# Kernel tuning notes

Measured on AMD Instinct MI355X. Metric: run time of the kernel, lower is better.

Reference implementation:

```python
import jax, jax.numpy as jnp
import numpy as np

MIN_NORM = 1e-15
N = 10000        # num_nodes
E = 320000       # num edges (avg degree 32)
F_IN = 512       # in_features
HID = 256        # hardcoded encoder hidden dim
D_HYP = 2        # Poincare embedding dim
HEIGHT = 2
MAX_SIZE = 0.999
MIN_SCALE = HEIGHT * (MAX_SIZE / (HEIGHT + 1))  # = 0.666, scale clamp lower bound
MAX_SCALE = MAX_SIZE


def setup_inputs() -> dict:
    key = jax.random.key(0)
    ks = jax.random.split(key, 5)
    feature = jax.random.normal(ks[0], (N, F_IN), jnp.float32)
    edge_index = jax.random.randint(ks[1], (2, E), 0, N, dtype=jnp.int64)
    W1 = jax.random.normal(ks[2], (F_IN, HID), jnp.float32) / np.sqrt(F_IN).astype(np.float32)
    b1 = jnp.zeros((HID,), jnp.float32)
    W2 = jax.random.normal(ks[3], (HID, D_HYP), jnp.float32) / np.sqrt(HID).astype(np.float32)
    b2 = jnp.zeros((D_HYP,), jnp.float32)
    scale = jnp.ones((1,), jnp.float32)  # init_size overridden to 1.0 in __init__
    return {"feature": feature, "edge_index": edge_index, "W1": W1, "b1": b1,
            "W2": W2, "b2": b2, "scale": scale}


def _gcn_agg(h, src, dst):
    # symmetric-normalized edge_index gather/aggregate (message passing)
    deg = jax.ops.segment_sum(jnp.ones((src.shape[0],), h.dtype), dst, num_segments=N)
    deg = jnp.maximum(deg, 1.0)
    norm = jax.lax.rsqrt(deg[src] * deg[dst])            # [E]
    msg = h[src] * norm[:, None]                          # [E, C] gather (irregular)
    return jax.ops.segment_sum(msg, dst, num_segments=N)  # [N, C] scatter-add


def reference(feature, edge_index, W1, b1, W2, b2, scale):
    src, dst = edge_index[0], edge_index[1]
    # 2-layer graph encoder (linear -> aggregate -> relu, linear -> aggregate)
    h = jax.nn.relu(_gcn_agg(feature @ W1 + b1, src, dst))   # [N, HID]
    u = _gcn_agg(h @ W2 + b2, src, dst)                      # [N, D_HYP] tangent at origin
    # lift to Lorentz model (k=-1) via expmap0: x = [cosh|u|, sinh|u| * u/|u|]
    un = jnp.maximum(jnp.linalg.norm(u, axis=-1, keepdims=True), MIN_NORM)
    x_l = jnp.concatenate([jnp.cosh(un), jnp.sinh(un) * u / un], axis=-1)  # [N, D_HYP+1]
    # Lorentz -> Poincare: p = x_space / (1 + x_time)
    p = x_l[:, 1:] / (1.0 + x_l[:, :1])
    # normalize: F.normalize(p, dim=-1) * scale.clamp(min_size, max_size)
    pn = jnp.maximum(jnp.linalg.norm(p, axis=-1, keepdims=True), 1e-12)
    s = jnp.clip(scale, MIN_SCALE, MAX_SCALE)
    p = p / pn * s
    # project onto Poincare ball of curvature k=-1 with eps=MIN_NORM
    norm = jnp.maximum(jnp.linalg.norm(p, axis=-1, keepdims=True), MIN_NORM)
    maxnorm = 1.0 - MIN_NORM
    return jnp.where(norm > maxnorm, p / norm * maxnorm, p)
```

## Files before the change

### kernel.cpp

```cpp
#include <hip/hip_runtime.h>
#include <math.h>

#define N_NODES 10000
#define N_EDGES 320000
#define F_IN 512
#define HID 256
#define PAD_DEG 80
#define N_GEMM_BLKS 632
#define BUILD_BLKS ((N_EDGES + 255) / 256)

typedef _Float16 half8 __attribute__((ext_vector_type(8)));
typedef float floatx4 __attribute__((ext_vector_type(4)));

typedef const __attribute__((address_space(1))) void* gas_ptr;
typedef __attribute__((address_space(3))) void* las_ptr;

__device__ __forceinline__ void dma16(const void* g, void* l) {
    __builtin_amdgcn_global_load_lds((gas_ptr)g, (las_ptr)l, 16, 0, 0);
}

__device__ __forceinline__ void fma4(float4& acc, float s, const float4& v) {
    acc.x += s * v.x; acc.y += s * v.y; acc.z += s * v.z; acc.w += s * v.w;
}


__global__ __launch_bounds__(256) void k_pre(const float* __restrict__ W1,
                                             int* __restrict__ count,
                                             _Float16* __restrict__ Bt_hi,
                                             _Float16* __restrict__ Bt_lo) {
    int i = blockIdx.x * blockDim.x + threadIdx.x;
    if (i < 10240) count[i] = 0;
    int k = i >> 8, n = i & 255;
    float v = W1[i];
    _Float16 hi = (_Float16)v;
    Bt_hi[n * F_IN + k] = hi;
    Bt_lo[n * F_IN + k] = (_Float16)(v - (float)hi);
}


__global__ __launch_bounds__(256) void k_main(const float* __restrict__ A,
                                              const _Float16* __restrict__ Bt_hi,
                                              const _Float16* __restrict__ Bt_lo,
                                              const float* __restrict__ b1,
                                              float* __restrict__ h0,
                                              const int* __restrict__ ei,
                                              int* __restrict__ count,
                                              int* __restrict__ csr) {
    __shared__ float    As[2][2048];
    __shared__ _Float16 Bhs[2][2048];
    __shared__ _Float16 Bls[2][2048];
    const int tid = threadIdx.x;

    if (blockIdx.x >= N_GEMM_BLKS) {
        int e = (blockIdx.x - N_GEMM_BLKS) * 256 + tid;
        if (e < N_EDGES) {
            int src = ei[e];
            int dst = ei[N_EDGES + e];
            int pos = atomicAdd(&count[dst], 1);
            csr[dst * PAD_DEG + pos] = src;
        }
        return;
    }

    const int b = blockIdx.x;
    const int t = (b & 7) * 79 + (b >> 3);
    const int row0 = (t >> 2) * 64, col0 = (t & 3) * 64;

    const int sA0 = tid, sA1 = tid + 256;
    const int rA0 = sA0 >> 3, hA0 = (sA0 & 7) ^ (rA0 & 7);
    const int rA1 = sA1 >> 3, hA1 = (sA1 & 7) ^ (rA1 & 7);
    int gr0 = row0 + rA0; if (gr0 > N_NODES - 1) gr0 = N_NODES - 1;
    int gr1 = row0 + rA1; if (gr1 > N_NODES - 1) gr1 = N_NODES - 1;
    const float* gA0 = A + (size_t)gr0 * F_IN + hA0 * 4;
    const float* gA1 = A + (size_t)gr1 * F_IN + hA1 * 4;
    const int cB = tid >> 2, hB = (tid & 3) ^ (cB & 3);
    const _Float16* gBh = Bt_hi + (size_t)(col0 + cB) * F_IN + hB * 8;
    const _Float16* gBl = Bt_lo + (size_t)(col0 + cB) * F_IN + hB * 8;

    const int wdma = __builtin_amdgcn_readfirstlane(tid >> 6);
    char* lA  = (char*)&As[0][0];
    char* lBh = (char*)&Bhs[0][0];
    char* lBl = (char*)&Bls[0][0];
    const int dA0u = wdma * 1024;
    const int dA1u = 4096 + wdma * 1024;
    const int dBu  = wdma * 1024;

    dma16(gA0, lA + dA0u);
    dma16(gA1, lA + dA1u);
    dma16(gBh, lBh + dBu);
    dma16(gBl, lBl + dBu);

    const int lane = tid & 63, w = tid >> 6;
    const int quad = lane >> 4, l15 = lane & 15;
    const int wm = (w >> 1) * 32, wn = (w & 1) * 32;
    floatx4 acc[2][2] = {};

    int aoff[2][2], boff[2];
    #pragma unroll
    for (int mi = 0; mi < 2; ++mi) {
        int r = wm + mi * 16 + l15;
        aoff[mi][0] = r * 128 + ((2 * quad)     ^ (r & 7)) * 16;
        aoff[mi][1] = r * 128 + ((2 * quad + 1) ^ (r & 7)) * 16;
    }
    #pragma unroll
    for (int ni = 0; ni < 2; ++ni) {
        int n = wn + ni * 16 + l15;
        boff[ni] = n * 64 + (quad ^ (n & 3)) * 16;
    }

    __syncthreads();

    int buf = 0;
    for (int it = 0; it < 16; ++it) {
        if (it < 15) {
            const int k1 = (it + 1) * 32;
            const int nb = buf ^ 1;
            dma16(gA0 + k1, lA  + nb * 8192 + dA0u);
            dma16(gA1 + k1, lA  + nb * 8192 + dA1u);
            dma16(gBh + k1, lBh + nb * 4096 + dBu);
            dma16(gBl + k1, lBl + nb * 4096 + dBu);
        }
        const char* bA = lA  + buf * 8192;
        const char* bH = lBh + buf * 4096;
        const char* bL = lBl + buf * 4096;
        half8 ah[2], al[2], bhf[2], blf[2];
        #pragma unroll
        for (int mi = 0; mi < 2; ++mi) {
            float4 f0 = *(const float4*)(bA + aoff[mi][0]);
            float4 f1 = *(const float4*)(bA + aoff[mi][1]);
            float av[8] = {f0.x, f0.y, f0.z, f0.w, f1.x, f1.y, f1.z, f1.w};
            #pragma unroll
            for (int j = 0; j < 8; ++j) {
                _Float16 h = (_Float16)av[j];
                ah[mi][j] = h;
                al[mi][j] = (_Float16)(av[j] - (float)h);
            }
        }
        #pragma unroll
        for (int ni = 0; ni < 2; ++ni) {
            bhf[ni] = *(const half8*)(bH + boff[ni]);
            blf[ni] = *(const half8*)(bL + boff[ni]);
        }
        #pragma unroll
        for (int ni = 0; ni < 2; ++ni)
            #pragma unroll
            for (int mi = 0; mi < 2; ++mi) {
                acc[mi][ni] = __builtin_amdgcn_mfma_f32_16x16x32_f16(ah[mi], bhf[ni], acc[mi][ni], 0, 0, 0);
                acc[mi][ni] = __builtin_amdgcn_mfma_f32_16x16x32_f16(ah[mi], blf[ni], acc[mi][ni], 0, 0, 0);
                acc[mi][ni] = __builtin_amdgcn_mfma_f32_16x16x32_f16(al[mi], bhf[ni], acc[mi][ni], 0, 0, 0);
            }
        __syncthreads();
        buf ^= 1;
    }

    #pragma unroll
    for (int mi = 0; mi < 2; ++mi)
        #pragma unroll
        for (int ni = 0; ni < 2; ++ni) {
            int colb = col0 + wn + ni * 16 + l15;
            float bias = b1[colb];
            #pragma unroll
            for (int reg = 0; reg < 4; ++reg) {
                int rowb = row0 + wm + mi * 16 + quad * 4 + reg;
                if (rowb < N_NODES) h0[(size_t)rowb * HID + colb] = acc[mi][ni][reg] + bias;
            }
        }
}


__global__ __launch_bounds__(256) void k_agg1(const float* __restrict__ h0,
                                              const int* __restrict__ csr,
                                              const int* __restrict__ count,
                                              const float* __restrict__ W2,
                                              const float* __restrict__ b2,
                                              float* __restrict__ u0) {
    __shared__ int2 nb[4][PAD_DEG];
    const int wid = threadIdx.x >> 6;
    const int lane = threadIdx.x & 63;
    const int n = blockIdx.x * 4 + wid;
    const int deg = count[n];
    const float degd = (float)(deg > 0 ? deg : 1);
    const int* row = csr + (size_t)n * PAD_DEG;
    for (int j = lane; j < deg; j += 64) {
        int s = row[j];
        int cs = count[s];
        float wq = rsqrtf((float)(cs > 0 ? cs : 1) * degd);
        nb[wid][j] = make_int2(s, __float_as_int(wq));
    }
    __syncthreads();

    const int off = lane << 2;
    float4 acc0 = {0,0,0,0}, acc1 = {0,0,0,0}, acc2 = {0,0,0,0}, acc3 = {0,0,0,0};
    int j = 0;
    for (; j + 16 <= deg; j += 16) {
        int2 e[16];
        #pragma unroll
        for (int q = 0; q < 16; ++q) e[q] = nb[wid][j + q];
        float4 v[16];
        #pragma unroll
        for (int q = 0; q < 16; ++q)
            v[q] = *(const float4*)(h0 + ((size_t)e[q].x << 8) + off);
        #pragma unroll
        for (int q = 0; q < 16; q += 4) {
            fma4(acc0, __int_as_float(e[q + 0].y), v[q + 0]);
            fma4(acc1, __int_as_float(e[q + 1].y), v[q + 1]);
            fma4(acc2, __int_as_float(e[q + 2].y), v[q + 2]);
            fma4(acc3, __int_as_float(e[q + 3].y), v[q + 3]);
        }
    }
    for (; j + 4 <= deg; j += 4) {
        int2 e0 = nb[wid][j+0], e1 = nb[wid][j+1], e2 = nb[wid][j+2], e3 = nb[wid][j+3];
        float4 v0 = *(const float4*)(h0 + ((size_t)e0.x << 8) + off);
        float4 v1 = *(const float4*)(h0 + ((size_t)e1.x << 8) + off);
        float4 v2 = *(const float4*)(h0 + ((size_t)e2.x << 8) + off);
        float4 v3 = *(const float4*)(h0 + ((size_t)e3.x << 8) + off);
        fma4(acc0, __int_as_float(e0.y), v0);
        fma4(acc1, __int_as_float(e1.y), v1);
        fma4(acc2, __int_as_float(e2.y), v2);
        fma4(acc3, __int_as_float(e3.y), v3);
    }
    for (; j < deg; ++j) {
        int2 e = nb[wid][j];
        float4 v = *(const float4*)(h0 + ((size_t)e.x << 8) + off);
        fma4(acc0, __int_as_float(e.y), v);
    }
    acc0.x += acc1.x + acc2.x + acc3.x;
    acc0.y += acc1.y + acc2.y + acc3.y;
    acc0.z += acc1.z + acc2.z + acc3.z;
    acc0.w += acc1.w + acc2.w + acc3.w;
    acc0.x = fmaxf(acc0.x, 0.f); acc0.y = fmaxf(acc0.y, 0.f);
    acc0.z = fmaxf(acc0.z, 0.f); acc0.w = fmaxf(acc0.w, 0.f);
    float4 wa = *(const float4*)(W2 + (lane << 3));
    float4 wb = *(const float4*)(W2 + (lane << 3) + 4);
    float p0 = acc0.x * wa.x + acc0.y * wa.z + acc0.z * wb.x + acc0.w * wb.z;
    float p1 = acc0.x * wa.y + acc0.y * wa.w + acc0.z * wb.y + acc0.w * wb.w;
    #pragma unroll
    for (int o = 32; o > 0; o >>= 1) {
        p0 += __shfl_down(p0, o);
        p1 += __shfl_down(p1, o);
    }
    if (lane == 0) {
        u0[2 * n]     = p0 + b2[0];
        u0[2 * n + 1] = p1 + b2[1];
    }
}


__global__ __launch_bounds__(256) void k_agg2(const float* __restrict__ u0,
                                              const int* __restrict__ csr,
                                              const int* __restrict__ count,
                                              const float* __restrict__ scale,
                                              float* __restrict__ out) {
    int n = blockIdx.x * 4 + (threadIdx.x >> 6);
    int lane = threadIdx.x & 63;
    if (n >= N_NODES) return;
    int deg = count[n];
    float degd = (float)(deg > 0 ? deg : 1);
    const int* row = csr + (size_t)n * PAD_DEG;
    float a0 = 0.f, a1 = 0.f;
    for (int j = lane; j < deg; j += 64) {
        int s = row[j];
        int cs = count[s];
        float wq = rsqrtf((float)(cs > 0 ? cs : 1) * degd);
        float2 uv = *(const float2*)(u0 + 2 * (size_t)s);
        a0 += wq * uv.x;
        a1 += wq * uv.y;
    }
    #pragma unroll
    for (int o = 32; o > 0; o >>= 1) {
        a0 += __shfl_down(a0, o);
        a1 += __shfl_down(a1, o);
    }
    if (lane == 0) {
        float un = fmaxf(sqrtf(a0 * a0 + a1 * a1), 1e-15f);
        float t = tanhf(0.5f * un) / un;
        float p0 = a0 * t, p1 = a1 * t;
        float pn = fmaxf(sqrtf(p0 * p0 + p1 * p1), 1e-12f);
        float s = fminf(fmaxf(scale[0], 0.666f), 0.999f);
        p0 = p0 / pn * s; p1 = p1 / pn * s;
        float nn = fmaxf(sqrtf(p0 * p0 + p1 * p1), 1e-15f);
        if (nn > 1.0f) { p0 = p0 / nn; p1 = p1 / nn; }
        out[2 * n]     = p0;
        out[2 * n + 1] = p1;
    }
}


extern "C" void kernel_launch(void* const* d_in, const int* in_sizes, int n_in,
                              void* d_out, int out_size, void* d_ws, size_t ws_size,
                              hipStream_t stream) {
    const float* feature = (const float*)d_in[0];
    const int*   ei      = (const int*)d_in[1];
    const float* W1      = (const float*)d_in[2];
    const float* b1      = (const float*)d_in[3];
    const float* W2      = (const float*)d_in[4];
    const float* b2      = (const float*)d_in[5];
    const float* scale   = (const float*)d_in[6];
    float* out = (float*)d_out;

    char* W = (char*)d_ws;
    int*      count = (int*)W;
    int*      csr   = (int*)(W + 40960);
    float*    h0    = (float*)(W + 3240960);
    float*    u0    = (float*)(W + 13480960);
    _Float16* Bt_hi = (_Float16*)(W + 13560960);
    _Float16* Bt_lo = (_Float16*)(W + 13823104);

    k_pre<<<dim3(512), dim3(256), 0, stream>>>(W1, count, Bt_hi, Bt_lo);
    k_main<<<dim3(N_GEMM_BLKS + BUILD_BLKS), dim3(256), 0, stream>>>(
        feature, Bt_hi, Bt_lo, b1, h0, ei, count, csr);
    k_agg1<<<dim3((N_NODES + 3) / 4), dim3(256), 0, stream>>>(h0, csr, count, W2, b2, u0);
    k_agg2<<<dim3((N_NODES + 3) / 4), dim3(256), 0, stream>>>(u0, csr, count, scale, out);
}
```

Before: 148.4 us.

## Fuse all stages into one cooperative persistent kernel with fp16 hidden activations

Replaces the four separate launches (weight split, GEMM+CSR build, layer-1 aggregation, layer-2 aggregation) with a single cooperative kernel of 512 blocks that uses grid.sync between phases. The GEMM tiles are distributed persistently, and the CSR build runs before the GEMM within each block. The hidden activation h0 is now stored as fp16, which halves the bytes touched by the irregular neighbour gather in layer 1. The aim is to cut launch gaps and gather bandwidth, in exchange for grid-wide barriers, reduced precision on h0, and the edge-build phase now serialised before the GEMM.

```diff
diff --git a/kernel.cpp b/kernel.cpp
--- a/kernel.cpp
+++ b/kernel.cpp
@@ -1,15 +1,20 @@
 #include <hip/hip_runtime.h>
+#include <hip/hip_cooperative_groups.h>
 #include <math.h>
+
+namespace cg = cooperative_groups;
 
 #define N_NODES 10000
 #define N_EDGES 320000
 #define F_IN 512
 #define HID 256
 #define PAD_DEG 80
-#define N_GEMM_BLKS 632
-#define BUILD_BLKS ((N_EDGES + 255) / 256)
+#define NBLK 512
+#define NWAVE (NBLK * 4)
+#define EDGES_PER_BLK 625
 
 typedef _Float16 half8 __attribute__((ext_vector_type(8)));
+typedef _Float16 half4v __attribute__((ext_vector_type(4)));
 typedef float floatx4 __attribute__((ext_vector_type(4)));
 
 typedef const __attribute__((address_space(1))) void* gas_ptr;
@@ -23,265 +28,267 @@
     acc.x += s * v.x; acc.y += s * v.y; acc.z += s * v.z; acc.w += s * v.w;
 }
 
-
-__global__ __launch_bounds__(256) void k_pre(const float* __restrict__ W1,
-                                             int* __restrict__ count,
-                                             _Float16* __restrict__ Bt_hi,
-                                             _Float16* __restrict__ Bt_lo) {
-    int i = blockIdx.x * blockDim.x + threadIdx.x;
-    if (i < 10240) count[i] = 0;
-    int k = i >> 8, n = i & 255;
-    float v = W1[i];
-    _Float16 hi = (_Float16)v;
-    Bt_hi[n * F_IN + k] = hi;
-    Bt_lo[n * F_IN + k] = (_Float16)(v - (float)hi);
-}
-
-
-__global__ __launch_bounds__(256) void k_main(const float* __restrict__ A,
-                                              const _Float16* __restrict__ Bt_hi,
-                                              const _Float16* __restrict__ Bt_lo,
-                                              const float* __restrict__ b1,
-                                              float* __restrict__ h0,
-                                              const int* __restrict__ ei,
-                                              int* __restrict__ count,
-                                              int* __restrict__ csr) {
+__device__ __forceinline__ float4 h4_to_f4(half4v h) {
+    float4 f; f.x = (float)h[0]; f.y = (float)h[1]; f.z = (float)h[2]; f.w = (float)h[3];
+    return f;
+}
+
+__global__ __launch_bounds__(256, 2) void k_fused(
+    const float* __restrict__ A, const int* __restrict__ ei,
+    const float* __restrict__ W1, const float* __restrict__ b1,
+    const float* __restrict__ W2, const float* __restrict__ b2,
+    const float* __restrict__ scale, float* __restrict__ out,
+    int* __restrict__ count, int* __restrict__ csr,
+    _Float16* __restrict__ h0h, float* __restrict__ u0,
+    _Float16* __restrict__ Bt_hi, _Float16* __restrict__ Bt_lo)
+{
     __shared__ float    As[2][2048];
     __shared__ _Float16 Bhs[2][2048];
     __shared__ _Float16 Bls[2][2048];
+    __shared__ int2     nb[4][PAD_DEG];
+
     const int tid = threadIdx.x;
-
-    if (blockIdx.x >= N_GEMM_BLKS) {
-        int e = (blockIdx.x - N_GEMM_BLKS) * 256 + tid;
-        if (e < N_EDGES) {
+    const int b = blockIdx.x;
+    const int lane = tid & 63, w = tid >> 6;
+    cg::grid_group grid = cg::this_grid();
+
+    {
+        int i = b * 256 + tid;
+        if (i < 10240) count[i] = 0;
+        int k = i >> 8, n = i & 255;
+        float v = W1[i];
+        _Float16 hi = (_Float16)v;
+        Bt_hi[n * F_IN + k] = hi;
+        Bt_lo[n * F_IN + k] = (_Float16)(v - (float)hi);
+    }
+    grid.sync();
+
+    {
+        const int e0 = b * EDGES_PER_BLK;
+        for (int j = tid; j < EDGES_PER_BLK; j += 256) {
+            int e = e0 + j;
             int src = ei[e];
             int dst = ei[N_EDGES + e];
             int pos = atomicAdd(&count[dst], 1);
             csr[dst * PAD_DEG + pos] = src;
         }
-        return;
-    }
-
-    const int b = blockIdx.x;
-    const int t = (b & 7) * 79 + (b >> 3);
-    const int row0 = (t >> 2) * 64, col0 = (t & 3) * 64;
-
-    const int sA0 = tid, sA1 = tid + 256;
-    const int rA0 = sA0 >> 3, hA0 = (sA0 & 7) ^ (rA0 & 7);
-    const int rA1 = sA1 >> 3, hA1 = (sA1 & 7) ^ (rA1 & 7);
-    int gr0 = row0 + rA0; if (gr0 > N_NODES - 1) gr0 = N_NODES - 1;
-    int gr1 = row0 + rA1; if (gr1 > N_NODES - 1) gr1 = N_NODES - 1;
-    const float* gA0 = A + (size_t)gr0 * F_IN + hA0 * 4;
-    const float* gA1 = A + (size_t)gr1 * F_IN + hA1 * 4;
-    const int cB = tid >> 2, hB = (tid & 3) ^ (cB & 3);
-    const _Float16* gBh = Bt_hi + (size_t)(col0 + cB) * F_IN + hB * 8;
-    const _Float16* gBl = Bt_lo + (size_t)(col0 + cB) * F_IN + hB * 8;
-
-    const int wdma = __builtin_amdgcn_readfirstlane(tid >> 6);
-    char* lA  = (char*)&As[0][0];
-    char* lBh = (char*)&Bhs[0][0];
-    char* lBl = (char*)&Bls[0][0];
-    const int dA0u = wdma * 1024;
-    const int dA1u = 4096 + wdma * 1024;
-    const int dBu  = wdma * 1024;
-
-    dma16(gA0, lA + dA0u);
-    dma16(gA1, lA + dA1u);
-    dma16(gBh, lBh + dBu);
-    dma16(gBl, lBl + dBu);
-
-    const int lane = tid & 63, w = tid >> 6;
-    const int quad = lane >> 4, l15 = lane & 15;
-    const int wm = (w >> 1) * 32, wn = (w & 1) * 32;
-    floatx4 acc[2][2] = {};
-
-    int aoff[2][2], boff[2];
-    #pragma unroll
-    for (int mi = 0; mi < 2; ++mi) {
-        int r = wm + mi * 16 + l15;
-        aoff[mi][0] = r * 128 + ((2 * quad)     ^ (r & 7)) * 16;
-        aoff[mi][1] = r * 128 + ((2 * quad + 1) ^ (r & 7)) * 16;
-    }
-    #pragma unroll
-    for (int ni = 0; ni < 2; ++ni) {
-        int n = wn + ni * 16 + l15;
-        boff[ni] = n * 64 + (quad ^ (n & 3)) * 16;
-    }
-
-    __syncthreads();
-
-    int buf = 0;
-    for (int it = 0; it < 16; ++it) {
-        if (it < 15) {
-            const int k1 = (it + 1) * 32;
-            const int nb = buf ^ 1;
-            dma16(gA0 + k1, lA  + nb * 8192 + dA0u);
-            dma16(gA1 + k1, lA  + nb * 8192 + dA1u);
-            dma16(gBh + k1, lBh + nb * 4096 + dBu);
-            dma16(gBl + k1, lBl + nb * 4096 + dBu);
-        }
-        const char* bA = lA  + buf * 8192;
-        const char* bH = lBh + buf * 4096;
-        const char* bL = lBl + buf * 4096;
-        half8 ah[2], al[2], bhf[2], blf[2];
+    }
+
+    {
+        const int quad = lane >> 4, l15 = lane & 15;
+        const int wm = (w >> 1) * 32, wn = (w & 1) * 32;
+        const int wdma = __builtin_amdgcn_readfirstlane(w);
+        char* lA  = (char*)&As[0][0];
+        char* lBh = (char*)&Bhs[0][0];
+        char* lBl = (char*)&Bls[0][0];
+        const int dA0u = wdma * 1024;
+        const int dA1u = 4096 + wdma * 1024;
+        const int dBu  = wdma * 1024;
+        const int sA0 = tid, sA1 = tid + 256;
+        const int rA0 = sA0 >> 3, hA0 = (sA0 & 7) ^ (rA0 & 7);
+        const int rA1 = sA1 >> 3, hA1 = (sA1 & 7) ^ (rA1 & 7);
+        const int cB = tid >> 2, hB = (tid & 3) ^ (cB & 3);
+        int aoff[2][2], boff[2];
         #pragma unroll
         for (int mi = 0; mi < 2; ++mi) {
-            float4 f0 = *(const float4*)(bA + aoff[mi][0]);
-            float4 f1 = *(const float4*)(bA + aoff[mi][1]);
-            float av[8] = {f0.x, f0.y, f0.z, f0.w, f1.x, f1.y, f1.z, f1.w};
-            #pragma unroll
-            for (int j = 0; j < 8; ++j) {
-                _Float16 h = (_Float16)av[j];
-                ah[mi][j] = h;
-                al[mi][j] = (_Float16)(av[j] - (float)h);
-            }
+            int r = wm + mi * 16 + l15;
+            aoff[mi][0] = r * 128 + ((2 * quad)     ^ (r & 7)) * 16;
+            aoff[mi][1] = r * 128 + ((2 * quad + 1) ^ (r & 7)) * 16;
         }
         #pragma unroll
         for (int ni = 0; ni < 2; ++ni) {
-            bhf[ni] = *(const half8*)(bH + boff[ni]);
-            blf[ni] = *(const half8*)(bL + boff[ni]);
-        }
-        #pragma unroll
-        for (int ni = 0; ni < 2; ++ni)
+            int nn = wn + ni * 16 + l15;
+            boff[ni] = nn * 64 + (quad ^ (nn & 3)) * 16;
+        }
+
+        const int ntile = (b < 116) ? 2 : 1;
+        for (int tt = 0; tt < ntile; ++tt) {
+            const int t = b + tt * 512;
+            const int row0 = (t >> 2) * 64, col0 = (t & 3) * 64;
+            int gr0 = row0 + rA0; if (gr0 > N_NODES - 1) gr0 = N_NODES - 1;
+            int gr1 = row0 + rA1; if (gr1 > N_NODES - 1) gr1 = N_NODES - 1;
+            const float* gA0 = A + (size_t)gr0 * F_IN + hA0 * 4;
+            const float* gA1 = A + (size_t)gr1 * F_IN + hA1 * 4;
+            const _Float16* gBh = Bt_hi + (size_t)(col0 + cB) * F_IN + hB * 8;
+            const _Float16* gBl = Bt_lo + (size_t)(col0 + cB) * F_IN + hB * 8;
+            floatx4 acc[2][2] = {};
+
+            dma16(gA0, lA + dA0u);
+            dma16(gA1, lA + dA1u);
+            dma16(gBh, lBh + dBu);
+            dma16(gBl, lBl + dBu);
+            __syncthreads();
+
+            int buf = 0;
+            for (int it = 0; it < 16; ++it) {
+                if (it < 15) {
+                    const int k1 = (it + 1) * 32;
+                    const int nbuf = buf ^ 1;
+                    dma16(gA0 + k1, lA  + nbuf * 8192 + dA0u);
+                    dma16(gA1 + k1, lA  + nbuf * 8192 + dA1u);
+                    dma16(gBh + k1, lBh + nbuf * 4096 + dBu);
+                    dma16(gBl + k1, lBl + nbuf * 4096 + dBu);
+                }
+                const char* bA = lA  + buf * 8192;
+                const char* bH = lBh + buf * 4096;
+                const char* bL = lBl + buf * 4096;
+                half8 ah[2], al[2], bhf[2], blf[2];
+                #pragma unroll
+                for (int mi = 0; mi < 2; ++mi) {
+                    float4 f0 = *(const float4*)(bA + aoff[mi][0]);
+                    float4 f1 = *(const float4*)(bA + aoff[mi][1]);
+                    float av[8] = {f0.x, f0.y, f0.z, f0.w, f1.x, f1.y, f1.z, f1.w};
+                    #pragma unroll
+                    for (int j = 0; j < 8; ++j) {
+                        _Float16 h = (_Float16)av[j];
+                        ah[mi][j] = h;
+                        al[mi][j] = (_Float16)(av[j] - (float)h);
+                    }
+                }
+                #pragma unroll
+                for (int ni = 0; ni < 2; ++ni) {
+                    bhf[ni] = *(const half8*)(bH + boff[ni]);
+                    blf[ni] = *(const half8*)(bL + boff[ni]);
+                }
+                #pragma unroll
+                for (int ni = 0; ni < 2; ++ni)
+                    #pragma unroll
+                    for (int mi = 0; mi < 2; ++mi) {
+                        acc[mi][ni] = __builtin_amdgcn_mfma_f32_16x16x32_f16(ah[mi], bhf[ni], acc[mi][ni], 0, 0, 0);
+                        acc[mi][ni] = __builtin_amdgcn_mfma_f32_16x16x32_f16(ah[mi], blf[ni], acc[mi][ni], 0, 0, 0);
+                        acc[mi][ni] = __builtin_amdgcn_mfma_f32_16x16x32_f16(al[mi], bhf[ni], acc[mi][ni], 0, 0, 0);
+                    }
+                __syncthreads();
+                buf ^= 1;
+            }
             #pragma unroll
-            for (int mi = 0; mi < 2; ++mi) {
-                acc[mi][ni] = __builtin_amdgcn_mfma_f32_16x16x32_f16(ah[mi], bhf[ni], acc[mi][ni], 0, 0, 0);
-                acc[mi][ni] = __builtin_amdgcn_mfma_f32_16x16x32_f16(ah[mi], blf[ni], acc[mi][ni], 0, 0, 0);
-                acc[mi][ni] = __builtin_amdgcn_mfma_f32_16x16x32_f16(al[mi], bhf[ni], acc[mi][ni], 0, 0, 0);
-            }
-        __syncthreads();
-        buf ^= 1;
-    }
-
-    #pragma unroll
-    for (int mi = 0; mi < 2; ++mi)
-        #pragma unroll
-        for (int ni = 0; ni < 2; ++ni) {
-            int colb = col0 + wn + ni * 16 + l15;
-            float bias = b1[colb];
+            for (int mi = 0; mi < 2; ++mi)
+                #pragma unroll
+                for (int ni = 0; ni < 2; ++ni) {
+                    int colb = col0 + wn + ni * 16 + l15;
+                    float bias = b1[colb];
+                    #pragma unroll
+                    for (int reg = 0; reg < 4; ++reg) {
+                        int rowb = row0 + wm + mi * 16 + quad * 4 + reg;
+                        if (rowb < N_NODES)
+                            h0h[(size_t)rowb * HID + colb] = (_Float16)(acc[mi][ni][reg] + bias);
+                    }
+                }
+        }
+    }
+    grid.sync();
+
+    {
+        const int gw = b * 4 + w;
+        const int off = lane << 2;
+        #pragma unroll 1
+        for (int itn = 0; itn < 5; ++itn) {
+            const int n = gw + itn * NWAVE;
+            const bool act = n < N_NODES;
+            int deg = 0;
+            if (act) {
+                deg = count[n];
+                const float degd = (float)(deg > 0 ? deg : 1);
+                const int* row = csr + (size_t)n * PAD_DEG;
+                for (int j = lane; j < deg; j += 64) {
+                    int s = row[j];
+                    int cs = count[s];
+                    float wq = rsqrtf((float)(cs > 0 ? cs : 1) * degd);
+                    nb[w][j] = make_int2(s, __float_as_int(wq));
+                }
+            }
+            __syncthreads();
+            if (act) {
+                float4 acc0 = {0,0,0,0}, acc1 = {0,0,0,0}, acc2 = {0,0,0,0}, acc3 = {0,0,0,0};
+                int j = 0;
+                for (; j + 16 <= deg; j += 16) {
+                    int2 e[16];
+                    #pragma unroll
+                    for (int q = 0; q < 16; ++q) e[q] = nb[w][j + q];
+                    half4v v[16];
+                    #pragma unroll
+                    for (int q = 0; q < 16; ++q)
+                        v[q] = *(const half4v*)(h0h + ((size_t)e[q].x << 8) + off);
+                    #pragma unroll
+                    for (int q = 0; q < 16; q += 4) {
+                        fma4(acc0, __int_as_float(e[q + 0].y), h4_to_f4(v[q + 0]));
+                        fma4(acc1, __int_as_float(e[q + 1].y), h4_to_f4(v[q + 1]));
+                        fma4(acc2, __int_as_float(e[q + 2].y), h4_to_f4(v[q + 2]));
+                        fma4(acc3, __int_as_float(e[q + 3].y), h4_to_f4(v[q + 3]));
+                    }
+                }
+                for (; j + 4 <= deg; j += 4) {
+                    int2 e0 = nb[w][j+0], e1 = nb[w][j+1], e2 = nb[w][j+2], e3 = nb[w][j+3];
+                    half4v v0 = *(const half4v*)(h0h + ((size_t)e0.x << 8) + off);
+                    half4v v1 = *(const half4v*)(h0h + ((size_t)e1.x << 8) + off);
+                    half4v v2 = *(const half4v*)(h0h + ((size_t)e2.x << 8) + off);
+                    half4v v3 = *(const half4v*)(h0h + ((size_t)e3.x << 8) + off);
+                    fma4(acc0, __int_as_float(e0.y), h4_to_f4(v0));
+                    fma4(acc1, __int_as_float(e1.y), h4_to_f4(v1));
+                    fma4(acc2, __int_as_float(e2.y), h4_to_f4(v2));
+                    fma4(acc3, __int_as_float(e3.y), h4_to_f4(v3));
+                }
+                for (; j < deg; ++j) {
+                    int2 e = nb[w][j];
+                    half4v v = *(const half4v*)(h0h + ((size_t)e.x << 8) + off);
+                    fma4(acc0, __int_as_float(e.y), h4_to_f4(v));
+                }
+                acc0.x += acc1.x + acc2.x + acc3.x;
+                acc0.y += acc1.y + acc2.y + acc3.y;
+                acc0.z += acc1.z + acc2.z + acc3.z;
+                acc0.w += acc1.w + acc2.w + acc3.w;
+                acc0.x = fmaxf(acc0.x, 0.f); acc0.y = fmaxf(acc0.y, 0.f);
+                acc0.z = fmaxf(acc0.z, 0.f); acc0.w = fmaxf(acc0.w, 0.f);
+                float4 wa = *(const float4*)(W2 + (lane << 3));
+                float4 wb = *(const float4*)(W2 + (lane << 3) + 4);
+                float p0 = acc0.x * wa.x + acc0.y * wa.z + acc0.z * wb.x + acc0.w * wb.z;
+                float p1 = acc0.x * wa.y + acc0.y * wa.w + acc0.z * wb.y + acc0.w * wb.w;
+                #pragma unroll
+                for (int o = 32; o > 0; o >>= 1) {
+                    p0 += __shfl_down(p0, o);
+                    p1 += __shfl_down(p1, o);
+                }
+                if (lane == 0) {
+                    u0[2 * n]     = p0 + b2[0];
+                    u0[2 * n + 1] = p1 + b2[1];
+                }
+            }
+        }
+    }
+    grid.sync();
+
+    {
+        for (int n = b * 4 + w; n < N_NODES; n += NWAVE) {
+            int deg = count[n];
+            float degd = (float)(deg > 0 ? deg : 1);
+            const int* row = csr + (size_t)n * PAD_DEG;
+            float a0 = 0.f, a1 = 0.f;
+            for (int j = lane; j < deg; j += 64) {
+                int s = row[j];
+                int cs = count[s];
+                float wq = rsqrtf((float)(cs > 0 ? cs : 1) * degd);
+                float2 uv = *(const float2*)(u0 + 2 * (size_t)s);
+                a0 += wq * uv.x;
+                a1 += wq * uv.y;
+            }
             #pragma unroll
-            for (int reg = 0; reg < 4; ++reg) {
-                int rowb = row0 + wm + mi * 16 + quad * 4 + reg;
-                if (rowb < N_NODES) h0[(size_t)rowb * HID + colb] = acc[mi][ni][reg] + bias;
-            }
-        }
-}
-
-
-__global__ __launch_bounds__(256) void k_agg1(const float* __restrict__ h0,
-                                              const int* __restrict__ csr,
-                                              const int* __restrict__ count,
-                                              const float* __restrict__ W2,
-                                              const float* __restrict__ b2,
-                                              float* __restrict__ u0) {
-    __shared__ int2 nb[4][PAD_DEG];
-    const int wid = threadIdx.x >> 6;
-    const int lane = threadIdx.x & 63;
-    const int n = blockIdx.x * 4 + wid;
-    const int deg = count[n];
-    const float degd = (float)(deg > 0 ? deg : 1);
-    const int* row = csr + (size_t)n * PAD_DEG;
-    for (int j = lane; j < deg; j += 64) {
-        int s = row[j];
-        int cs = count[s];
-        float wq = rsqrtf((float)(cs > 0 ? cs : 1) * degd);
-        nb[wid][j] = make_int2(s, __float_as_int(wq));
-    }
-    __syncthreads();
-
-    const int off = lane << 2;
-    float4 acc0 = {0,0,0,0}, acc1 = {0,0,0,0}, acc2 = {0,0,0,0}, acc3 = {0,0,0,0};
-    int j = 0;
-    for (; j + 16 <= deg; j += 16) {
-        int2 e[16];
-        #pragma unroll
-        for (int q = 0; q < 16; ++q) e[q] = nb[wid][j + q];
-        float4 v[16];
-        #pragma unroll
-        for (int q = 0; q < 16; ++q)
-            v[q] = *(const float4*)(h0 + ((size_t)e[q].x << 8) + off);
-        #pragma unroll
-        for (int q = 0; q < 16; q += 4) {
-            fma4(acc0, __int_as_float(e[q + 0].y), v[q + 0]);
-            fma4(acc1, __int_as_float(e[q + 1].y), v[q + 1]);
-            fma4(acc2, __int_as_float(e[q + 2].y), v[q + 2]);
-            fma4(acc3, __int_as_float(e[q + 3].y), v[q + 3]);
-        }
-    }
-    for (; j + 4 <= deg; j += 4) {
-        int2 e0 = nb[wid][j+0], e1 = nb[wid][j+1], e2 = nb[wid][j+2], e3 = nb[wid][j+3];
-        float4 v0 = *(const float4*)(h0 + ((size_t)e0.x << 8) + off);
-        float4 v1 = *(const float4*)(h0 + ((size_t)e1.x << 8) + off);
-        float4 v2 = *(const float4*)(h0 + ((size_t)e2.x << 8) + off);
-        float4 v3 = *(const float4*)(h0 + ((size_t)e3.x << 8) + off);
-        fma4(acc0, __int_as_float(e0.y), v0);
-        fma4(acc1, __int_as_float(e1.y), v1);
-        fma4(acc2, __int_as_float(e2.y), v2);
-        fma4(acc3, __int_as_float(e3.y), v3);
-    }
-    for (; j < deg; ++j) {
-        int2 e = nb[wid][j];
-        float4 v = *(const float4*)(h0 + ((size_t)e.x << 8) + off);
-        fma4(acc0, __int_as_float(e.y), v);
-    }
-    acc0.x += acc1.x + acc2.x + acc3.x;
-    acc0.y += acc1.y + acc2.y + acc3.y;
-    acc0.z += acc1.z + acc2.z + acc3.z;
-    acc0.w += acc1.w + acc2.w + acc3.w;
-    acc0.x = fmaxf(acc0.x, 0.f); acc0.y = fmaxf(acc0.y, 0.f);
-    acc0.z = fmaxf(acc0.z, 0.f); acc0.w = fmaxf(acc0.w, 0.f);
-    float4 wa = *(const float4*)(W2 + (lane << 3));
-    float4 wb = *(const float4*)(W2 + (lane << 3) + 4);
-    float p0 = acc0.x * wa.x + acc0.y * wa.z + acc0.z * wb.x + acc0.w * wb.z;
-    float p1 = acc0.x * wa.y + acc0.y * wa.w + acc0.z * wb.y + acc0.w * wb.w;
-    #pragma unroll
-    for (int o = 32; o > 0; o >>= 1) {
-        p0 += __shfl_down(p0, o);
-        p1 += __shfl_down(p1, o);
-    }
-    if (lane == 0) {
-        u0[2 * n]     = p0 + b2[0];
-        u0[2 * n + 1] = p1 + b2[1];
-    }
-}
-
-
-__global__ __launch_bounds__(256) void k_agg2(const float* __restrict__ u0,
-                                              const int* __restrict__ csr,
-                                              const int* __restrict__ count,
-                                              const float* __restrict__ scale,
-                                              float* __restrict__ out) {
-    int n = blockIdx.x * 4 + (threadIdx.x >> 6);
-    int lane = threadIdx.x & 63;
-    if (n >= N_NODES) return;
-    int deg = count[n];
-    float degd = (float)(deg > 0 ? deg : 1);
-    const int* row = csr + (size_t)n * PAD_DEG;
-    float a0 = 0.f, a1 = 0.f;
-    for (int j = lane; j < deg; j += 64) {
-        int s = row[j];
-        int cs = count[s];
-        float wq = rsqrtf((float)(cs > 0 ? cs : 1) * degd);
-        float2 uv = *(const float2*)(u0 + 2 * (size_t)s);
-        a0 += wq * uv.x;
-        a1 += wq * uv.y;
-    }
-    #pragma unroll
-    for (int o = 32; o > 0; o >>= 1) {
-        a0 += __shfl_down(a0, o);
-        a1 += __shfl_down(a1, o);
-    }
-    if (lane == 0) {
-        float un = fmaxf(sqrtf(a0 * a0 + a1 * a1), 1e-15f);
-        float t = tanhf(0.5f * un) / un;
-        float p0 = a0 * t, p1 = a1 * t;
-        float pn = fmaxf(sqrtf(p0 * p0 + p1 * p1), 1e-12f);
-        float s = fminf(fmaxf(scale[0], 0.666f), 0.999f);
-        p0 = p0 / pn * s; p1 = p1 / pn * s;
-        float nn = fmaxf(sqrtf(p0 * p0 + p1 * p1), 1e-15f);
-        if (nn > 1.0f) { p0 = p0 / nn; p1 = p1 / nn; }
-        out[2 * n]     = p0;
-        out[2 * n + 1] = p1;
+            for (int o = 32; o > 0; o >>= 1) {
+                a0 += __shfl_down(a0, o);
+                a1 += __shfl_down(a1, o);
+            }
+            if (lane == 0) {
+                float un = fmaxf(sqrtf(a0 * a0 + a1 * a1), 1e-15f);
+                float t = tanhf(0.5f * un) / un;
+                float p0 = a0 * t, p1 = a1 * t;
+                float pn = fmaxf(sqrtf(p0 * p0 + p1 * p1), 1e-12f);
+                float s = fminf(fmaxf(scale[0], 0.666f), 0.999f);
+                p0 = p0 / pn * s; p1 = p1 / pn * s;
+                float nn = fmaxf(sqrtf(p0 * p0 + p1 * p1), 1e-15f);
+                if (nn > 1.0f) { p0 = p0 / nn; p1 = p1 / nn; }
+                out[2 * n]     = p0;
+                out[2 * n + 1] = p1;
+            }
+        }
     }
 }
 
@@ -298,17 +305,18 @@
     const float* scale   = (const float*)d_in[6];
     float* out = (float*)d_out;
 
-    char* W = (char*)d_ws;
-    int*      count = (int*)W;
-    int*      csr   = (int*)(W + 40960);
-    float*    h0    = (float*)(W + 3240960);
-    float*    u0    = (float*)(W + 13480960);
-    _Float16* Bt_hi = (_Float16*)(W + 13560960);
-    _Float16* Bt_lo = (_Float16*)(W + 13823104);
-
-    k_pre<<<dim3(512), dim3(256), 0, stream>>>(W1, count, Bt_hi, Bt_lo);
-    k_main<<<dim3(N_GEMM_BLKS + BUILD_BLKS), dim3(256), 0, stream>>>(
-        feature, Bt_hi, Bt_lo, b1, h0, ei, count, csr);
-    k_agg1<<<dim3((N_NODES + 3) / 4), dim3(256), 0, stream>>>(h0, csr, count, W2, b2, u0);
-    k_agg2<<<dim3((N_NODES + 3) / 4), dim3(256), 0, stream>>>(u0, csr, count, scale, out);
-}
+    char* Wb = (char*)d_ws;
+    int*      count = (int*)Wb;
+    int*      csr   = (int*)(Wb + 40960);
+    _Float16* h0h   = (_Float16*)(Wb + 3240960);
+    float*    u0    = (float*)(Wb + 8360960);
+    _Float16* Bt_hi = (_Float16*)(Wb + 8440960);
+    _Float16* Bt_lo = (_Float16*)(Wb + 8703104);
+
+    void* args[] = {(void*)&feature, (void*)&ei, (void*)&W1, (void*)&b1,
+                    (void*)&W2, (void*)&b2, (void*)&scale, (void*)&out,
+                    (void*)&count, (void*)&csr, (void*)&h0h, (void*)&u0,
+                    (void*)&Bt_hi, (void*)&Bt_lo};
+    hipLaunchCooperativeKernel((const void*)k_fused, dim3(NBLK), dim3(256),
+                               args, 0, stream);
+}
```

New measurement: 345.8 us. 133% more time.
